# Kernel optimization log

Hardware: AMD Instinct MI355X
Metric: run time of the kernel (lower is better)

## Reference

```python
import jax, jax.numpy as jnp
import numpy as np

BETA = 0.25


def setup_inputs() -> dict:
    key = jax.random.key(0)
    k1, k2 = jax.random.split(key)
    z_e = jax.random.normal(k1, (32, 256, 32, 32), dtype=jnp.float32)
    embedding = jax.random.normal(k2, (1024, 256), dtype=jnp.float32)
    return {"z_e": z_e, "embedding": embedding}


def reference(z_e, embedding):
    B, D, H, W = z_e.shape  # (32, 256, 32, 32)
    K = embedding.shape[0]
    # flatten to (N, D), N = B*H*W
    z_flat = jnp.transpose(z_e, (0, 2, 3, 1)).reshape(-1, D)
    # squared L2 distances: ||z||^2 + ||e||^2 - 2 z.e^T  -> (N, K)
    dist = (
        jnp.sum(z_flat * z_flat, axis=1, keepdims=True)
        + jnp.sum(embedding * embedding, axis=1)
        - 2.0 * z_flat @ embedding.T
    )
    codes = jnp.argmin(dist, axis=1)  # (N,) int
    # gather codebook vectors, reshape back to (B, D, H, W)
    z_q = embedding[codes].reshape(B, H, W, D).transpose(0, 3, 1, 2)
    # commitment loss (mse over all elements)
    sg = jax.lax.stop_gradient
    commit_loss = (
        jnp.mean((sg(z_q) - z_e) ** 2)
        + BETA * jnp.mean((z_q - sg(z_e)) ** 2)
    )
    # straight-through estimator
    z_q_st = z_e + sg(z_q - z_e)
    return z_q_st, codes.reshape(B, H, W), commit_loss
```

## Files before the change

kernel.cpp:

```cpp
#include <hip/hip_runtime.h>

typedef _Float16 f16;
typedef __attribute__((ext_vector_type(4))) _Float16 f16x4;
typedef __attribute__((ext_vector_type(8))) _Float16 f16x8;
typedef __attribute__((ext_vector_type(4))) float f32x4;

#define D_DIM 256
#define K_CB  1024
#define N_TOT 32768
#define DHW   262144
#define ZQ_N  8388608
#define OUT_CODES 8388608
#define OUT_LOSS  8421376

#define WS_BSP   0
#define WS_EN2   131072
#define WS_CODES 132096
#define WS_CNT   164864
#define WS_LIST  164928
#define WS_RLOSS 197696
#define LIST_CAP 32768
#define EPS_GAP  0.08f

__global__ void vq_prep(const float* __restrict__ emb, float* __restrict__ ws) {
    const int k = blockIdx.x;
    const int t = threadIdx.x;
    const float4 v = *reinterpret_cast<const float4*>(emb + k * D_DIM + t * 4);
    float s = v.x * v.x + v.y * v.y + v.z * v.z + v.w * v.w;
#pragma unroll
    for (int off = 32; off > 0; off >>= 1) s += __shfl_down(s, off);
    if (t == 0) ws[WS_EN2 + k] = -0.5f * s;
    const float a[4] = {v.x, v.y, v.z, v.w};
    f16x4 hv;
#pragma unroll
    for (int i = 0; i < 4; ++i) hv[i] = (f16)a[i];
    *reinterpret_cast<f16x4*>(reinterpret_cast<f16*>(ws) + k * 256 + t * 4) = hv;
    if (k == 0 && t == 0) reinterpret_cast<int*>(ws + WS_CNT)[0] = 0;
}

__global__ __launch_bounds__(256, 2) void vq_gemm(const float* __restrict__ z,
                                                  float* ws,
                                                  float* __restrict__ out) {
    __shared__ __align__(16) char lds[66560];
    f16* Ahi = reinterpret_cast<f16*>(lds);
    f16* Bs  = reinterpret_cast<f16*>(lds + 32768);
    float* rowsum = reinterpret_cast<float*>(lds + 65536);
    float* comb = reinterpret_cast<float*>(lds + 32768);

    const f16* __restrict__ Bsp = reinterpret_cast<const f16*>(ws);
    const float* __restrict__ en2 = ws + WS_EN2;
    const int tid = threadIdx.x;
    const int lane = tid & 63;
    const int w = tid >> 6;
    const int r0 = blockIdx.x * 64;
    const float* __restrict__ zb = z + (r0 >> 10) * DHW + (r0 & 1023);

    {
        const int arow = tid & 63;
        const int adg  = tid >> 6;
        float sq = 0.f;
#pragma unroll
        for (int p = 0; p < 16; ++p) {
            const int d = adg * 64 + p * 4;
            f16x4 hv;
#pragma unroll
            for (int i = 0; i < 4; ++i) {
                const float x = zb[(d + i) * 1024 + arow];
                hv[i] = (f16)x;
                sq += x * x;
            }
            const int byte = (arow * 512 + d * 2) ^ ((arow & 7) << 4);
            *reinterpret_cast<f16x4*>(reinterpret_cast<char*>(Ahi) + byte) = hv;
        }
        rowsum[adg * 64 + arow] = sq;
    }

    float bv[16], sv[16];
    int   bk[16];
#pragma unroll
    for (int i = 0; i < 16; ++i) { bv[i] = -3.0e38f; sv[i] = -3.0e38f; bk[i] = 0; }

    f32x4 acc[4][4];
#pragma unroll
    for (int i = 0; i < 4; ++i)
#pragma unroll
        for (int j = 0; j < 4; ++j) acc[i][j] = f32x4{0.f, 0.f, 0.f, 0.f};

    f16x8 breg[8];
#pragma unroll
    for (int p = 0; p < 8; ++p) {
        const int u = tid + p * 256;
        breg[p] = *reinterpret_cast<const f16x8*>(Bsp + (u >> 3) * 256 + (u & 7) * 8);
    }
    float e2v[4];

    for (int q = 0; q < 16; ++q) {
        __syncthreads();
#pragma unroll
        for (int p = 0; p < 8; ++p) {
            const int u = tid + p * 256;
            const int col = u >> 3, k8 = (u & 7) * 8;
            const int byte = (col * 128 + k8 * 2) ^ ((col & 7) << 4);
            *reinterpret_cast<f16x8*>(reinterpret_cast<char*>(Bs) + byte) = breg[p];
        }
        if ((q & 3) == 2) {
            const int c0 = (q >> 2) * 256;
#pragma unroll
            for (int jf = 0; jf < 4; ++jf)
                e2v[jf] = en2[c0 + w * 64 + jf * 16 + (lane & 15)];
        }
        __syncthreads();
        if (q < 15) {
            const int qn = q + 1;
            const int c0n = (qn >> 2) * 256, kbn = (qn & 3) * 64;
#pragma unroll
            for (int p = 0; p < 8; ++p) {
                const int u = tid + p * 256;
                breg[p] = *reinterpret_cast<const f16x8*>(
                    Bsp + (c0n + (u >> 3)) * 256 + kbn + (u & 7) * 8);
            }
        }
        const int kA = (q & 3) * 64;
#pragma unroll
        for (int s = 0; s < 2; ++s) {
            const int kl = s * 32 + (lane >> 4) * 8;
            f16x8 bf[4], af[4];
#pragma unroll
            for (int jf = 0; jf < 4; ++jf) {
                const int col = w * 64 + jf * 16 + (lane & 15);
                bf[jf] = *reinterpret_cast<const f16x8*>(
                    reinterpret_cast<const char*>(Bs) +
                    ((col * 128 + kl * 2) ^ ((col & 7) << 4)));
            }
#pragma unroll
            for (int i = 0; i < 4; ++i) {
                const int row = i * 16 + (lane & 15);
                af[i] = *reinterpret_cast<const f16x8*>(
                    reinterpret_cast<const char*>(Ahi) +
                    ((row * 512 + (kA + kl) * 2) ^ ((row & 7) << 4)));
            }
#pragma unroll
            for (int i = 0; i < 4; ++i)
#pragma unroll
                for (int jf = 0; jf < 4; ++jf)
                    acc[i][jf] = __builtin_amdgcn_mfma_f32_16x16x32_f16(
                        af[i], bf[jf], acc[i][jf], 0, 0, 0);
        }
        if ((q & 3) == 3) {
            const int c0 = (q >> 2) * 256;
#pragma unroll
            for (int jf = 0; jf < 4; ++jf) {
                const int col = c0 + w * 64 + jf * 16 + (lane & 15);
                const float e2 = e2v[jf];
#pragma unroll
                for (int i = 0; i < 4; ++i)
#pragma unroll
                    for (int r = 0; r < 4; ++r) {
                        const float v = acc[i][jf][r] + e2;
                        const int idx = i * 4 + r;
                        if (v > bv[idx]) { sv[idx] = bv[idx]; bv[idx] = v; bk[idx] = col; }
                        else if (v > sv[idx]) sv[idx] = v;
                    }
            }
#pragma unroll
            for (int i = 0; i < 4; ++i)
#pragma unroll
                for (int j = 0; j < 4; ++j) acc[i][j] = f32x4{0.f, 0.f, 0.f, 0.f};
        }
    }

#pragma unroll
    for (int m = 1; m <= 8; m <<= 1)
#pragma unroll
        for (int idx = 0; idx < 16; ++idx) {
            const float pv = __shfl_xor(bv[idx], m);
            const float ps = __shfl_xor(sv[idx], m);
            const int   pk = __shfl_xor(bk[idx], m);
            if (pv > bv[idx] || (pv == bv[idx] && pk < bk[idx])) {
                sv[idx] = fmaxf(bv[idx], ps);
                bv[idx] = pv; bk[idx] = pk;
            } else {
                sv[idx] = fmaxf(sv[idx], pv);
            }
        }

    __syncthreads();
    if ((lane & 15) == 0) {
#pragma unroll
        for (int idx = 0; idx < 16; ++idx) {
            const int row = (idx >> 2) * 16 + (lane >> 4) * 4 + (idx & 3);
            comb[(w * 64 + row) * 3 + 0] = bv[idx];
            comb[(w * 64 + row) * 3 + 1] = sv[idx];
            comb[(w * 64 + row) * 3 + 2] = __int_as_float(bk[idx]);
        }
    }
    __syncthreads();
    if (tid < 64) {
        const int row = tid;
        float bvf = comb[row * 3 + 0], svf = comb[row * 3 + 1];
        int   bkf = __float_as_int(comb[row * 3 + 2]);
#pragma unroll
        for (int q2 = 1; q2 < 4; ++q2) {
            const float v = comb[(q2 * 64 + row) * 3 + 0];
            const float s2 = comb[(q2 * 64 + row) * 3 + 1];
            const int   k2 = __float_as_int(comb[(q2 * 64 + row) * 3 + 2]);
            if (v > bvf) { svf = fmaxf(bvf, s2); bvf = v; bkf = k2; }
            else         { svf = fmaxf(svf, v); }
        }
        const int n = r0 + row;
        reinterpret_cast<int*>(ws + WS_CODES)[n] = bkf;
        out[OUT_CODES + n] = (float)bkf;
        const float znorm = rowsum[row] + rowsum[64 + row] +
                            rowsum[128 + row] + rowsum[192 + row];
        ws[WS_RLOSS + n] = znorm - 2.f * bvf;
        if (bvf - svf < EPS_GAP) {
            const int pos = atomicAdd(reinterpret_cast<int*>(ws + WS_CNT), 1);
            if (pos < LIST_CAP) reinterpret_cast<int*>(ws + WS_LIST)[pos] = n;
        }
    }
}

__global__ __launch_bounds__(256) void vq_rescore(const float* __restrict__ z,
                                                  const float* __restrict__ emb,
                                                  float* ws,
                                                  float* __restrict__ out) {
    __shared__ float zl[256];
    __shared__ float zred[4];
    __shared__ float rv[4];
    __shared__ int   rk[4];
    const int cnt0 = reinterpret_cast<const int*>(ws + WS_CNT)[0];
    const int cnt = cnt0 < LIST_CAP ? cnt0 : LIST_CAP;
    const int t = threadIdx.x;
    for (int it = blockIdx.x; it < cnt; it += gridDim.x) {
        const int n = reinterpret_cast<const int*>(ws + WS_LIST)[it];
        const int b = n >> 10, hw = n & 1023;
        __syncthreads();
        const float x = z[b * DHW + t * 1024 + hw];
        zl[t] = x;
        float zs = x * x;
#pragma unroll
        for (int off = 32; off > 0; off >>= 1) zs += __shfl_down(zs, off);
        if ((t & 63) == 0) zred[t >> 6] = zs;
        __syncthreads();
        float bvv = -3.0e38f; int bkk = 0;
#pragma unroll
        for (int j = 0; j < 4; ++j) {
            const int k = t + j * 256;
            const float* e = emb + k * D_DIM;
            float dot = 0.f;
#pragma unroll 8
            for (int d = 0; d < 256; d += 4) {
                const float4 ev = *reinterpret_cast<const float4*>(e + d);
                const float4 zv = *reinterpret_cast<const float4*>(zl + d);
                dot += ev.x * zv.x + ev.y * zv.y + ev.z * zv.z + ev.w * zv.w;
            }
            const float v = dot + ws[WS_EN2 + k];
            if (v > bvv || (v == bvv && k < bkk)) { bvv = v; bkk = k; }
        }
#pragma unroll
        for (int m = 1; m <= 32; m <<= 1) {
            const float pv = __shfl_xor(bvv, m);
            const int   pk = __shfl_xor(bkk, m);
            if (pv > bvv || (pv == bvv && pk < bkk)) { bvv = pv; bkk = pk; }
        }
        if ((t & 63) == 0) { rv[t >> 6] = bvv; rk[t >> 6] = bkk; }
        __syncthreads();
        if (t == 0) {
#pragma unroll
            for (int q = 1; q < 4; ++q)
                if (rv[q] > bvv || (rv[q] == bvv && rk[q] < bkk)) { bvv = rv[q]; bkk = rk[q]; }
            reinterpret_cast<int*>(ws + WS_CODES)[n] = bkk;
            out[OUT_CODES + n] = (float)bkk;
            const float znorm = zred[0] + zred[1] + zred[2] + zred[3];
            ws[WS_RLOSS + n] = znorm - 2.f * bvv;
        }
    }
}

__global__ __launch_bounds__(256) void vq_gather(const float* __restrict__ emb,
                                                 float* ws,
                                                 float* __restrict__ out) {
    __shared__ __align__(16) float el[64][260];
    __shared__ int cl[64];
    const int tid = threadIdx.x;
    const int n0 = blockIdx.x * 64;
    const int b = n0 >> 10, hw0 = n0 & 1023;
    if (tid < 64) cl[tid] = reinterpret_cast<const int*>(ws + WS_CODES)[n0 + tid];
    __syncthreads();
#pragma unroll
    for (int p = 0; p < 16; ++p) {
        const int u = tid + p * 256;
        const int r = u >> 6, f4 = (u & 63) * 4;
        *reinterpret_cast<float4*>(&el[r][f4]) =
            *reinterpret_cast<const float4*>(emb + cl[r] * D_DIM + f4);
    }
    __syncthreads();
    const int hw4 = (tid & 15) * 4, dg = tid >> 4;
    float* op = out + b * DHW + hw0 + hw4;
#pragma unroll
    for (int dd = 0; dd < 16; ++dd) {
        const int d = dg * 16 + dd;
        float4 q;
        q.x = el[hw4 + 0][d]; q.y = el[hw4 + 1][d];
        q.z = el[hw4 + 2][d]; q.w = el[hw4 + 3][d];
        *reinterpret_cast<float4*>(op + d * 1024) = q;
    }
}

__global__ __launch_bounds__(256) void vq_finalize(const float* __restrict__ ws,
                                                   float* __restrict__ out) {
    __shared__ float red[4];
    const int t = threadIdx.x;
    const float4* rl = reinterpret_cast<const float4*>(ws + WS_RLOSS);
    float s = 0.f;
#pragma unroll
    for (int i = 0; i < 32; ++i) {
        const float4 v = rl[t + i * 256];
        s += v.x + v.y + v.z + v.w;
    }
#pragma unroll
    for (int off = 32; off > 0; off >>= 1) s += __shfl_down(s, off);
    if ((t & 63) == 0) red[t >> 6] = s;
    __syncthreads();
    if (t == 0)
        out[OUT_LOSS] = (red[0] + red[1] + red[2] + red[3]) * (1.25f / 8388608.0f);
}

extern "C" void kernel_launch(void* const* d_in, const int* in_sizes, int n_in,
                              void* d_out, int out_size, void* d_ws, size_t ws_size,
                              hipStream_t stream) {
    const float* z   = (const float*)d_in[0];
    const float* emb = (const float*)d_in[1];
    float* out = (float*)d_out;
    float* ws  = (float*)d_ws;

    vq_prep<<<K_CB, 64, 0, stream>>>(emb, ws);
    vq_gemm<<<N_TOT / 64, 256, 0, stream>>>(z, ws, out);
    vq_rescore<<<256, 256, 0, stream>>>(z, emb, ws, out);
    vq_gather<<<ZQ_N / (256 * 64), 256, 0, stream>>>(emb, ws, out);
    vq_finalize<<<1, 256, 0, stream>>>(ws, out);
}
```

Baseline: 218.1 us.

## Stream codebook fragments directly from global memory and reshape gather transpose

The GEMM kernel no longer stages codebook tiles in shared memory. Each wave now owns 256 codebook columns and loads its MFMA B fragments straight from global (L2-resident) memory with register double-buffering, which drops the per-step barriers and cuts LDS use so more blocks can share a CU. The gather kernel switches to scalar loads and stores through a padded 257-stride LDS tile to avoid bank conflicts, and the rescore launch doubles its grid. The risks are that global fragment loads are less coalesced and add latency, and that the gather now issues narrower stores.

```diff
diff --git a/kernel.cpp b/kernel.cpp
--- a/kernel.cpp
+++ b/kernel.cpp
@@ -41,17 +41,17 @@
 __global__ __launch_bounds__(256, 2) void vq_gemm(const float* __restrict__ z,
                                                   float* ws,
                                                   float* __restrict__ out) {
-    __shared__ __align__(16) char lds[66560];
+    __shared__ __align__(16) char lds[36864];
     f16* Ahi = reinterpret_cast<f16*>(lds);
-    f16* Bs  = reinterpret_cast<f16*>(lds + 32768);
-    float* rowsum = reinterpret_cast<float*>(lds + 65536);
-    float* comb = reinterpret_cast<float*>(lds + 32768);
+    float* rowsum = reinterpret_cast<float*>(lds + 32768);
+    float* comb   = reinterpret_cast<float*>(lds + 33792);
 
     const f16* __restrict__ Bsp = reinterpret_cast<const f16*>(ws);
     const float* __restrict__ en2 = ws + WS_EN2;
     const int tid = threadIdx.x;
     const int lane = tid & 63;
     const int w = tid >> 6;
+    const int cw = w * 256;
     const int r0 = blockIdx.x * 64;
     const float* __restrict__ zb = z + (r0 >> 10) * DHW + (r0 & 1023);
 
@@ -75,69 +75,53 @@
         rowsum[adg * 64 + arow] = sq;
     }
 
+    float e2r[16];
+#pragma unroll
+    for (int st = 0; st < 4; ++st)
+#pragma unroll
+        for (int jf = 0; jf < 4; ++jf)
+            e2r[st * 4 + jf] = en2[cw + st * 64 + jf * 16 + (lane & 15)];
+
+    __syncthreads();
+
     float bv[16], sv[16];
     int   bk[16];
 #pragma unroll
     for (int i = 0; i < 16; ++i) { bv[i] = -3.0e38f; sv[i] = -3.0e38f; bk[i] = 0; }
 
-    f32x4 acc[4][4];
-#pragma unroll
-    for (int i = 0; i < 4; ++i)
-#pragma unroll
-        for (int j = 0; j < 4; ++j) acc[i][j] = f32x4{0.f, 0.f, 0.f, 0.f};
-
-    f16x8 breg[8];
-#pragma unroll
-    for (int p = 0; p < 8; ++p) {
-        const int u = tid + p * 256;
-        breg[p] = *reinterpret_cast<const f16x8*>(Bsp + (u >> 3) * 256 + (u & 7) * 8);
-    }
-    float e2v[4];
-
-    for (int q = 0; q < 16; ++q) {
-        __syncthreads();
-#pragma unroll
-        for (int p = 0; p < 8; ++p) {
-            const int u = tid + p * 256;
-            const int col = u >> 3, k8 = (u & 7) * 8;
-            const int byte = (col * 128 + k8 * 2) ^ ((col & 7) << 4);
-            *reinterpret_cast<f16x8*>(reinterpret_cast<char*>(Bs) + byte) = breg[p];
-        }
-        if ((q & 3) == 2) {
-            const int c0 = (q >> 2) * 256;
-#pragma unroll
-            for (int jf = 0; jf < 4; ++jf)
-                e2v[jf] = en2[c0 + w * 64 + jf * 16 + (lane & 15)];
-        }
-        __syncthreads();
-        if (q < 15) {
-            const int qn = q + 1;
-            const int c0n = (qn >> 2) * 256, kbn = (qn & 3) * 64;
-#pragma unroll
-            for (int p = 0; p < 8; ++p) {
-                const int u = tid + p * 256;
-                breg[p] = *reinterpret_cast<const f16x8*>(
-                    Bsp + (c0n + (u >> 3)) * 256 + kbn + (u & 7) * 8);
-            }
-        }
-        const int kA = (q & 3) * 64;
-#pragma unroll
-        for (int s = 0; s < 2; ++s) {
-            const int kl = s * 32 + (lane >> 4) * 8;
-            f16x8 bf[4], af[4];
-#pragma unroll
-            for (int jf = 0; jf < 4; ++jf) {
-                const int col = w * 64 + jf * 16 + (lane & 15);
-                bf[jf] = *reinterpret_cast<const f16x8*>(
-                    reinterpret_cast<const char*>(Bs) +
-                    ((col * 128 + kl * 2) ^ ((col & 7) << 4)));
-            }
+    const f16* __restrict__ bptr = Bsp + (cw + (lane & 15)) * 256 + (lane >> 4) * 8;
+
+    f16x8 bf[4], bfn[4];
+#pragma unroll
+    for (int jf = 0; jf < 4; ++jf)
+        bf[jf] = *reinterpret_cast<const f16x8*>(bptr + (jf * 16) * 256);
+
+#pragma unroll
+    for (int st = 0; st < 4; ++st) {
+        f32x4 acc[4][4];
+#pragma unroll
+        for (int i = 0; i < 4; ++i)
+#pragma unroll
+            for (int j = 0; j < 4; ++j) acc[i][j] = f32x4{0.f, 0.f, 0.f, 0.f};
+
+#pragma unroll
+        for (int ks = 0; ks < 8; ++ks) {
+            const int nst = (ks == 7) ? st + 1 : st;
+            const int nks = (ks == 7) ? 0 : ks + 1;
+            if (nst < 4) {
+#pragma unroll
+                for (int jf = 0; jf < 4; ++jf)
+                    bfn[jf] = *reinterpret_cast<const f16x8*>(
+                        bptr + (nst * 64 + jf * 16) * 256 + nks * 32);
+            }
+            const int kk = ks * 32 + (lane >> 4) * 8;
+            f16x8 af[4];
 #pragma unroll
             for (int i = 0; i < 4; ++i) {
                 const int row = i * 16 + (lane & 15);
                 af[i] = *reinterpret_cast<const f16x8*>(
                     reinterpret_cast<const char*>(Ahi) +
-                    ((row * 512 + (kA + kl) * 2) ^ ((row & 7) << 4)));
+                    ((row * 512 + kk * 2) ^ ((row & 7) << 4)));
             }
 #pragma unroll
             for (int i = 0; i < 4; ++i)
@@ -145,27 +129,23 @@
                 for (int jf = 0; jf < 4; ++jf)
                     acc[i][jf] = __builtin_amdgcn_mfma_f32_16x16x32_f16(
                         af[i], bf[jf], acc[i][jf], 0, 0, 0);
-        }
-        if ((q & 3) == 3) {
-            const int c0 = (q >> 2) * 256;
-#pragma unroll
-            for (int jf = 0; jf < 4; ++jf) {
-                const int col = c0 + w * 64 + jf * 16 + (lane & 15);
-                const float e2 = e2v[jf];
-#pragma unroll
-                for (int i = 0; i < 4; ++i)
-#pragma unroll
-                    for (int r = 0; r < 4; ++r) {
-                        const float v = acc[i][jf][r] + e2;
-                        const int idx = i * 4 + r;
-                        if (v > bv[idx]) { sv[idx] = bv[idx]; bv[idx] = v; bk[idx] = col; }
-                        else if (v > sv[idx]) sv[idx] = v;
-                    }
-            }
+#pragma unroll
+            for (int jf = 0; jf < 4; ++jf) bf[jf] = bfn[jf];
+        }
+        const int c0 = cw + st * 64;
+#pragma unroll
+        for (int jf = 0; jf < 4; ++jf) {
+            const int col = c0 + jf * 16 + (lane & 15);
+            const float e2 = e2r[st * 4 + jf];
 #pragma unroll
             for (int i = 0; i < 4; ++i)
 #pragma unroll
-                for (int j = 0; j < 4; ++j) acc[i][j] = f32x4{0.f, 0.f, 0.f, 0.f};
+                for (int r = 0; r < 4; ++r) {
+                    const float v = acc[i][jf][r] + e2;
+                    const int idx = i * 4 + r;
+                    if (v > bv[idx]) { sv[idx] = bv[idx]; bv[idx] = v; bk[idx] = col; }
+                    else if (v > sv[idx]) sv[idx] = v;
+                }
         }
     }
 
@@ -184,7 +164,6 @@
             }
         }
 
-    __syncthreads();
     if ((lane & 15) == 0) {
 #pragma unroll
         for (int idx = 0; idx < 16; ++idx) {
@@ -201,7 +180,7 @@
         int   bkf = __float_as_int(comb[row * 3 + 2]);
 #pragma unroll
         for (int q2 = 1; q2 < 4; ++q2) {
-            const float v = comb[(q2 * 64 + row) * 3 + 0];
+            const float v  = comb[(q2 * 64 + row) * 3 + 0];
             const float s2 = comb[(q2 * 64 + row) * 3 + 1];
             const int   k2 = __float_as_int(comb[(q2 * 64 + row) * 3 + 2]);
             if (v > bvf) { svf = fmaxf(bvf, s2); bvf = v; bkf = k2; }
@@ -280,31 +259,23 @@
 __global__ __launch_bounds__(256) void vq_gather(const float* __restrict__ emb,
                                                  float* ws,
                                                  float* __restrict__ out) {
-    __shared__ __align__(16) float el[64][260];
+    __shared__ float el[64 * 257];
     __shared__ int cl[64];
     const int tid = threadIdx.x;
     const int n0 = blockIdx.x * 64;
     const int b = n0 >> 10, hw0 = n0 & 1023;
     if (tid < 64) cl[tid] = reinterpret_cast<const int*>(ws + WS_CODES)[n0 + tid];
     __syncthreads();
-#pragma unroll
-    for (int p = 0; p < 16; ++p) {
-        const int u = tid + p * 256;
-        const int r = u >> 6, f4 = (u & 63) * 4;
-        *reinterpret_cast<float4*>(&el[r][f4]) =
-            *reinterpret_cast<const float4*>(emb + cl[r] * D_DIM + f4);
-    }
-    __syncthreads();
-    const int hw4 = (tid & 15) * 4, dg = tid >> 4;
-    float* op = out + b * DHW + hw0 + hw4;
-#pragma unroll
-    for (int dd = 0; dd < 16; ++dd) {
-        const int d = dg * 16 + dd;
-        float4 q;
-        q.x = el[hw4 + 0][d]; q.y = el[hw4 + 1][d];
-        q.z = el[hw4 + 2][d]; q.w = el[hw4 + 3][d];
-        *reinterpret_cast<float4*>(op + d * 1024) = q;
-    }
+#pragma unroll 8
+    for (int p = 0; p < 64; ++p)
+        el[p * 257 + tid] = emb[cl[p] * D_DIM + tid];
+    __syncthreads();
+    const int hw = tid & 63, dg = tid >> 6;
+    float* op = out + b * DHW + hw0 + hw;
+    const float* erow = el + hw * 257 + dg * 64;
+#pragma unroll 8
+    for (int dd = 0; dd < 64; ++dd)
+        op[(dg * 64 + dd) * 1024] = erow[dd];
 }
 
 __global__ __launch_bounds__(256) void vq_finalize(const float* __restrict__ ws,
@@ -336,7 +307,7 @@
 
     vq_prep<<<K_CB, 64, 0, stream>>>(emb, ws);
     vq_gemm<<<N_TOT / 64, 256, 0, stream>>>(z, ws, out);
-    vq_rescore<<<256, 256, 0, stream>>>(z, emb, ws, out);
+    vq_rescore<<<512, 256, 0, stream>>>(z, emb, ws, out);
     vq_gather<<<ZQ_N / (256 * 64), 256, 0, stream>>>(emb, ws, out);
     vq_finalize<<<1, 256, 0, stream>>>(ws, out);
 }
```

New measurement: 222.0 us. About the same (+1.8%).
